# Kernel tuning notes

Hardware: AMD Instinct MI355X
Metric: run time of the kernel (lower is better)

## Reference

```python
import jax, jax.numpy as jnp
from jax import lax
import numpy as np

B, C, H, W = 8, 192, 56, 56
N = H * W
K_CLUSTERS = 16   # num_centroids
K_NBRS = 9        # kNN neighbors
FACTOR = 2
COUT = C * FACTOR # hidden channels of graph conv
CPE_K = 7         # depthwise CPE kernel (odd)


def setup_inputs() -> dict:
    key = jax.random.key(0)
    ks = jax.random.split(key, 12)
    s = 0.02
    return {
        "x": jax.random.normal(ks[0], (B, C, H, W), jnp.float32),
        "labels": jax.random.randint(ks[1], (B, N), 0, K_CLUSTERS, jnp.int32),
        "cpe_w": jax.random.normal(ks[2], (C, 1, CPE_K, CPE_K), jnp.float32) * s,
        "cpe_b": jnp.zeros((C,), jnp.float32),
        "fc1_w": jax.random.normal(ks[3], (C, C), jnp.float32) * s,
        "fc1_b": jnp.zeros((C,), jnp.float32),
        "nn_v_w": jax.random.normal(ks[4], (2 * C, COUT), jnp.float32) * s,
        "nn_v_b": jnp.zeros((COUT,), jnp.float32),
        "nn_c_w": jax.random.normal(ks[5], (2 * C, COUT), jnp.float32) * s,
        "nn_c_b": jnp.zeros((COUT,), jnp.float32),
        "fc2_w": jax.random.normal(ks[6], (COUT, C), jnp.float32) * s,
        "fc2_b": jnp.zeros((C,), jnp.float32),
    }


def reference(x, labels, cpe_w, cpe_b, fc1_w, fc1_b, nn_v_w, nn_v_b,
              nn_c_w, nn_c_b, fc2_w, fc2_b):
    Bx, Cx, Hx, Wx = x.shape
    n = Hx * Wx
    shortcut = x
    # --- Conditional Position Encoding: depthwise conv + residual ---
    pe = lax.conv_general_dilated(
        x, cpe_w, (1, 1), "SAME", feature_group_count=Cx,
        dimension_numbers=("NCHW", "OIHW", "NCHW"))
    x = pe + cpe_b[None, :, None, None] + x
    # --- fc1: 1x1 conv ---
    xf = jnp.einsum("bchw,cd->bdhw", x, fc1_w) + fc1_b[None, :, None, None]
    xn = xf.reshape(Bx, Cx, n).transpose(0, 2, 1)  # [B,N,C]
    # --- organize_and_map: stable sort nodes by cluster label ---
    order = jnp.argsort(labels, axis=1)            # sorted pos -> orig idx (stable)
    mapping = jnp.argsort(order, axis=1)           # orig idx -> sorted pos
    xs = jnp.take_along_axis(xn, order[:, :, None], axis=1)  # [B,N,C]
    ls = jnp.take_along_axis(labels, order, axis=1)          # [B,N]
    # --- kNN on l2-normalized feats, restricted to same cluster ---
    xe = xs / jnp.maximum(jnp.linalg.norm(xs, axis=-1, keepdims=True), 1e-12)
    sq = jnp.sum(xe * xe, axis=-1)                 # [B,N]
    d2 = sq[:, :, None] + sq[:, None, :] - 2.0 * jnp.einsum("bnc,bmc->bnm", xe, xe)
    same = ls[:, :, None] == ls[:, None, :]        # [B,N,N] cluster mask
    d2 = jnp.where(same, d2, jnp.inf)
    _, nbr = lax.top_k(-d2, K_NBRS)                # [B,N,k] nearest in-cluster
    valid = jnp.take_along_axis(same, nbr, axis=2) # False when cluster < k
    # --- vertex edge conv: max_j MLP([x_i, x_j - x_i]) ---
    xj = jax.vmap(lambda xb, nb: xb[nb])(xs, nbr)  # [B,N,k,C]
    xi = xs[:, :, None, :]
    msg = jnp.concatenate([jnp.broadcast_to(xi, xj.shape), xj - xi], axis=-1)
    h = jax.nn.gelu(msg @ nn_v_w + nn_v_b)         # [B,N,k,COUT]
    h = jnp.where(valid[..., None], h, -jnp.inf)   # self is always valid
    hv = jnp.max(h, axis=2)                        # [B,N,COUT]
    # --- centroid edge conv over cluster centers (fully connected per image) ---
    onehot = (ls[:, :, None] == jnp.arange(K_CLUSTERS)[None, None, :]).astype(xs.dtype)
    cnt = jnp.maximum(onehot.sum(axis=1), 1.0)     # [B,K]
    cen = jnp.einsum("bnk,bnc->bkc", onehot, xs) / cnt[:, :, None]
    ci = cen[:, :, None, :]
    cj = cen[:, None, :, :]
    cmsg = jnp.concatenate(
        [jnp.broadcast_to(ci, (Bx, K_CLUSTERS, K_CLUSTERS, Cx)), cj - ci], axis=-1)
    hc = jnp.max(jax.nn.gelu(cmsg @ nn_c_w + nn_c_b), axis=2)  # [B,K,COUT]
    hcn = jax.vmap(lambda hb, lb: hb[lb])(hc, ls)  # scatter center feat to nodes
    hn = hv + hcn                                  # [B,N,COUT]
    # --- unshuffle back to original raster order ---
    out_nodes = jnp.take_along_axis(hn, mapping[:, :, None], axis=1)
    # --- fc2: 1x1 conv back to C, residual ---
    y = out_nodes @ fc2_w + fc2_b                  # [B,N,C]
    y = y.transpose(0, 2, 1).reshape(Bx, Cx, Hx, Wx)
    return y + shortcut
```

## Files before the change

kernel.cpp:

```cpp
#include <hip/hip_runtime.h>
#include <math.h>

#define NB 8
#define NC 192
#define NH 56
#define NW 56
#define NN 3136
#define NK 16
#define KNB 9
#define NCOUT 384
#define LPMAX 320
#define DSTRIDE 320
#define DSLOT (320 * 320)

#define FLT_INF __builtin_inff()

typedef short s16x8 __attribute__((ext_vector_type(8)));
typedef _Float16 f16x8 __attribute__((ext_vector_type(8)));
typedef float f32x4 __attribute__((ext_vector_type(4)));
typedef unsigned short us8 __attribute__((ext_vector_type(8)));
typedef unsigned short us4 __attribute__((ext_vector_type(4)));

__device__ __forceinline__ float gelu_t(float x) {
    const float k0 = 0.7978845608028654f;
    float u = k0 * (x + 0.044715f * x * x * x);
    float sg = __builtin_amdgcn_rcpf(1.0f + __expf(-2.0f * u));
    return x * sg;
}

__device__ __forceinline__ unsigned short f2bf(float f) {
    unsigned u = __float_as_uint(f);
    u += 0x7fff + ((u >> 16) & 1);
    return (unsigned short)(u >> 16);
}

__device__ __forceinline__ float bf2f(unsigned short h) {
    return __uint_as_float(((unsigned)h) << 16);
}

#define FRONT_CONV_BLOCKS (NB * NC)
#define FRONT_ORDER_BLOCKS (NB * NK)
#define FRONT_WCVT_BLOCKS 288
__global__ __launch_bounds__(256) void front_kernel(
    const float* __restrict__ X, const float* __restrict__ W7, const float* __restrict__ bias,
    unsigned short* __restrict__ xpe,
    const int* __restrict__ labels, int* __restrict__ order, int* __restrict__ mapping,
    int* __restrict__ lsv, int* __restrict__ cntk, int* __restrict__ offk,
    const float* __restrict__ Wf1, const float* __restrict__ Wv, const float* __restrict__ Wf2,
    unsigned short* __restrict__ wf1, unsigned short* __restrict__ wfpmq,
    unsigned short* __restrict__ wfq, unsigned short* __restrict__ wf2) {
    __shared__ float tile[62 * 62];
    __shared__ float wl[49];
    int bid = blockIdx.x;
    int tid = threadIdx.x;
    if (bid < FRONT_CONV_BLOCKS) {
        int bc = bid;
        int c = bc % NC;
        const float* Xp = X + (size_t)bc * NN;
        if (tid < 49) wl[tid] = W7[(size_t)c * 49 + tid];
        for (int idx = tid; idx < 62 * 62; idx += 256) {
            int ty = idx / 62, tx = idx % 62;
            int gy = ty - 3, gx = tx - 3;
            float v = 0.0f;
            if (gy >= 0 && gy < NH && gx >= 0 && gx < NW) v = Xp[gy * NW + gx];
            tile[idx] = v;
        }
        __syncthreads();
        float cb = bias[c];
        for (int g = tid; g < (NN / 4); g += 256) {
            int y = g / (NW / 4), x0 = (g % (NW / 4)) * 4;
            float a0 = 0.f, a1 = 0.f, a2 = 0.f, a3 = 0.f;
#pragma unroll
            for (int dy = 0; dy < 7; ++dy) {
                const float* tr = &tile[(y + dy) * 62 + x0];
#pragma unroll
                for (int dx = 0; dx < 7; ++dx) {
                    float wv = wl[dy * 7 + dx];
                    a0 += tr[dx] * wv;
                    a1 += tr[dx + 1] * wv;
                    a2 += tr[dx + 2] * wv;
                    a3 += tr[dx + 3] * wv;
                }
            }
            const float* rr = &tile[(y + 3) * 62 + x0 + 3];
            us4 o;
            o[0] = f2bf(a0 + cb + rr[0]);
            o[1] = f2bf(a1 + cb + rr[1]);
            o[2] = f2bf(a2 + cb + rr[2]);
            o[3] = f2bf(a3 + cb + rr[3]);
            *(us4*)(xpe + (size_t)bc * NN + y * NW + x0) = o;
        }
    } else if (bid < FRONT_CONV_BLOCKS + FRONT_ORDER_BLOCKS) {
        if (tid >= 64) return;
        int idx = bid - FRONT_CONV_BLOCKS;
        int b = idx >> 4;
        int k = idx & 15;
        int lane = tid;
        const int* lb = labels + (size_t)b * NN;
        int cntLess = 0, cntEq = 0;
        for (int n0 = 0; n0 < NN; n0 += 64) {
            int lab = lb[n0 + lane] & 15;
            cntLess += __popcll(__ballot(lab < k));
            cntEq += __popcll(__ballot(lab == k));
        }
        int base = cntLess;
        int run = 0;
        for (int n0 = 0; n0 < NN; n0 += 64) {
            int n = n0 + lane;
            int lab = lb[n] & 15;
            bool p = (lab == k);
            unsigned long long mask = __ballot(p);
            int rank = __popcll(mask & ((1ull << lane) - 1ull));
            if (p) {
                int pos = base + run + rank;
                order[b * NN + pos] = n;
                mapping[b * NN + n] = pos;
                lsv[b * NN + pos] = k;
            }
            run += __popcll(mask);
        }
        if (lane == 0) {
            offk[b * NK + k] = base;
            cntk[b * NK + k] = cntEq;
        }
    } else {
        int u = bid - (FRONT_CONV_BLOCKS + FRONT_ORDER_BLOCKS);
        int nt = u % 6, kc = (u / 6) % 12, z = u / 72;
        const float* W;
        unsigned short* Bf;
        int ldw, rowoff, KC, NT;
        bool diff = false;
        if (z == 0) { W = Wf1; Bf = wf1; ldw = NC; rowoff = 0; KC = 6; NT = 3; }
        else if (z == 1) { W = Wv; Bf = wfpmq; ldw = NCOUT; rowoff = 0; KC = 6; NT = 6; diff = true; }
        else if (z == 2) { W = Wv; Bf = wfq; ldw = NCOUT; rowoff = NC; KC = 6; NT = 6; }
        else { W = Wf2; Bf = wf2; ldw = NC; rowoff = 0; KC = 12; NT = 3; }
        if (nt >= NT || kc >= KC) return;
        int c = tid >> 6, l = tid & 63;
        int n = l & 15, q = l >> 4;
        int col = nt * 64 + c * 16 + n;
        int krow = rowoff + kc * 32 + q * 8;
        unsigned short pack[8];
#pragma unroll
        for (int j = 0; j < 8; ++j) {
            float v = W[(size_t)(krow + j) * ldw + col];
            if (diff) v -= W[(size_t)(NC + krow + j) * ldw + col];
            pack[j] = f2bf(v);
        }
        *(us8*)(Bf + ((((size_t)nt * KC + kc) * 4 + c) * 64 + l) * 8) = *(const us8*)pack;
    }
}

__global__ __launch_bounds__(256) void tcvt_kernel(const unsigned short* __restrict__ xpe,
                                                   unsigned short* __restrict__ Af) {
    __shared__ unsigned short t[32][72];
    int b = blockIdx.z, kc = blockIdx.y, n0 = blockIdx.x * 64;
    int tid = threadIdx.x;
    int cl = tid >> 3, nl = (tid & 7) * 8;
    const unsigned short* src = xpe + ((size_t)b * NC + kc * 32 + cl) * NN + n0 + nl;
    *(us8*)&t[cl][nl] = *(const us8*)src;
    __syncthreads();
    int w = tid >> 6, l = tid & 63;
    int m = l & 15, q = l >> 4;
    int nloc = w * 16 + m;
    unsigned short pack[8];
#pragma unroll
    for (int j = 0; j < 8; ++j) pack[j] = t[q * 8 + j][nloc];
    int sg = blockIdx.x * 4 + w;
    *(us8*)(Af + (size_t)b * NN * NC + (((size_t)sg * 6 + kc) * 64 + l) * 8) =
        *(const us8*)pack;
}

template <int KC>
__global__ __launch_bounds__(256) void gemm_mfma(const unsigned short* __restrict__ Af,
                                                 size_t aStride,
                                                 const unsigned short* __restrict__ Bf,
                                                 const float* __restrict__ bias,
                                                 float* __restrict__ C, size_t cStride,
                                                 int ldc, unsigned short* __restrict__ Cfrag,
                                                 const int* __restrict__ rowmap) {
    int b = blockIdx.z;
    int w = threadIdx.x >> 6, lane = threadIdx.x & 63;
    int sg = blockIdx.y * 4 + w;
    int n0 = blockIdx.x * 64;
    const unsigned short* Ap = Af + (size_t)b * aStride + ((size_t)sg * KC * 64 + lane) * 8;
    const unsigned short* Bp = Bf + ((size_t)blockIdx.x * KC * 256 + lane) * 8;
    f32x4 acc[4] = {};
#pragma unroll
    for (int kc = 0; kc < KC; ++kc) {
        s16x8 a = *(const s16x8*)(Ap + kc * 512);
#pragma unroll
        for (int c = 0; c < 4; ++c) {
            s16x8 bv = *(const s16x8*)(Bp + kc * 2048 + c * 512);
            acc[c] = __builtin_amdgcn_mfma_f32_16x16x32_bf16(a, bv, acc[c], 0, 0, 0);
        }
    }
    int col0 = lane & 15, rq = lane >> 4;
    float* Cb = C + (size_t)b * cStride;
    int kcd = ldc >> 5;
#pragma unroll
    for (int r = 0; r < 4; ++r) {
        int grow = sg * 16 + rq * 4 + r;
        int orow = rowmap ? rowmap[(size_t)b * NN + grow] : grow;
#pragma unroll
        for (int c = 0; c < 4; ++c) {
            int col = n0 + c * 16 + col0;
            float v = acc[c][r];
            if (bias) v += bias[col];
            Cb[(size_t)orow * ldc + col] = v;
            if (Cfrag) {
                int s2 = orow >> 4, m2 = orow & 15;
                int kc2 = col >> 5, q2 = (col >> 3) & 3, j2 = col & 7;
                Cfrag[(size_t)b * cStride +
                      (((size_t)s2 * kcd + kc2) * 64 + q2 * 16 + m2) * 8 + j2] = f2bf(v);
            }
        }
    }
}

template <int KC>
__global__ __launch_bounds__(256) void gemm_mfma_pq(const unsigned short* __restrict__ Af,
                                                    size_t aStride,
                                                    const unsigned short* __restrict__ B1,
                                                    const unsigned short* __restrict__ B2,
                                                    const float* __restrict__ bias,
                                                    unsigned short* __restrict__ PmQ,
                                                    unsigned short* __restrict__ Qh,
                                                    size_t cStride, int ldc) {
    int b = blockIdx.z;
    int w = threadIdx.x >> 6, lane = threadIdx.x & 63;
    int sg = blockIdx.y * 4 + w;
    int n0 = blockIdx.x * 64;
    const unsigned short* Ap = Af + (size_t)b * aStride + ((size_t)sg * KC * 64 + lane) * 8;
    const unsigned short* Bp1 = B1 + ((size_t)blockIdx.x * KC * 256 + lane) * 8;
    const unsigned short* Bp2 = B2 + ((size_t)blockIdx.x * KC * 256 + lane) * 8;
    f32x4 acc1[4] = {};
    f32x4 acc2[4] = {};
#pragma unroll
    for (int kc = 0; kc < KC; ++kc) {
        s16x8 a = *(const s16x8*)(Ap + kc * 512);
#pragma unroll
        for (int c = 0; c < 4; ++c) {
            s16x8 b1 = *(const s16x8*)(Bp1 + kc * 2048 + c * 512);
            acc1[c] = __builtin_amdgcn_mfma_f32_16x16x32_bf16(a, b1, acc1[c], 0, 0, 0);
            s16x8 b2 = *(const s16x8*)(Bp2 + kc * 2048 + c * 512);
            acc2[c] = __builtin_amdgcn_mfma_f32_16x16x32_bf16(a, b2, acc2[c], 0, 0, 0);
        }
    }
    int col0 = lane & 15, rq = lane >> 4;
    unsigned short* Pb = PmQ + (size_t)b * cStride;
    unsigned short* Qb = Qh + (size_t)b * cStride;
#pragma unroll
    for (int r = 0; r < 4; ++r) {
        int grow = sg * 16 + rq * 4 + r;
#pragma unroll
        for (int c = 0; c < 4; ++c) {
            int col = n0 + c * 16 + col0;
            Pb[(size_t)grow * ldc + col] = f2bf(acc1[c][r] + bias[col]);
            Qb[(size_t)grow * ldc + col] = f2bf(acc2[c][r]);
        }
    }
}

template <int KC>
__global__ __launch_bounds__(256) void gemm_mfma_hb(const unsigned short* __restrict__ Af,
                                                    size_t aStride,
                                                    const unsigned short* __restrict__ Bf,
                                                    const float* __restrict__ bias,
                                                    unsigned short* __restrict__ C,
                                                    size_t cStride, int ldc,
                                                    const int* __restrict__ rowmap) {
    int b = blockIdx.z;
    int w = threadIdx.x >> 6, lane = threadIdx.x & 63;
    int sg = blockIdx.y * 4 + w;
    int n0 = blockIdx.x * 64;
    const unsigned short* Ap = Af + (size_t)b * aStride + ((size_t)sg * KC * 64 + lane) * 8;
    const unsigned short* Bp = Bf + ((size_t)blockIdx.x * KC * 256 + lane) * 8;
    f32x4 acc[4] = {};
#pragma unroll
    for (int kc = 0; kc < KC; ++kc) {
        s16x8 a = *(const s16x8*)(Ap + kc * 512);
#pragma unroll
        for (int c = 0; c < 4; ++c) {
            s16x8 bv = *(const s16x8*)(Bp + kc * 2048 + c * 512);
            acc[c] = __builtin_amdgcn_mfma_f32_16x16x32_bf16(a, bv, acc[c], 0, 0, 0);
        }
    }
    int col0 = lane & 15, rq = lane >> 4;
    unsigned short* Cb = C + (size_t)b * cStride;
#pragma unroll
    for (int r = 0; r < 4; ++r) {
        int grow = sg * 16 + rq * 4 + r;
        int orow = rowmap[(size_t)b * NN + grow];
#pragma unroll
        for (int c = 0; c < 4; ++c) {
            int col = n0 + c * 16 + col0;
            Cb[(size_t)orow * ldc + col] = f2bf(acc[c][r] + bias[col]);
        }
    }
}

__global__ __launch_bounds__(384) void xe_cvt_kernel(const float* __restrict__ xs,
                                                     const int* __restrict__ offk,
                                                     const int* __restrict__ cntk,
                                                     _Float16* __restrict__ xef,
                                                     float* __restrict__ sqv) {
    __shared__ float psum[16][25];
    __shared__ float rloc[16];
    int b = blockIdx.z, k = blockIdx.y, strip = blockIdx.x;
    int bk = b * NK + k;
    int base = offk[bk], L = cntk[bk];
    if (strip * 16 >= L) return;
    int kc = threadIdx.x >> 6, l = threadIdx.x & 63;
    int m = l & 15, q = l >> 4;
    int rl = strip * 16 + m;
    int row = base + (rl < L ? rl : L - 1);
    const float* src = xs + ((size_t)b * NN + row) * NC + kc * 32 + q * 8;
    float4 v0 = *(const float4*)src;
    float4 v1 = *(const float4*)(src + 4);
    float part = v0.x * v0.x + v0.y * v0.y + v0.z * v0.z + v0.w * v0.w + v1.x * v1.x +
                 v1.y * v1.y + v1.z * v1.z + v1.w * v1.w;
    psum[m][kc * 4 + q] = part;
    __syncthreads();
    if (threadIdx.x < 16) {
        float s = 0.0f;
#pragma unroll
        for (int i2 = 0; i2 < 24; ++i2) s += psum[threadIdx.x][i2];
        float nrm = fmaxf(sqrtf(s), 1e-12f);
        float ri = 1.0f / nrm;
        rloc[threadIdx.x] = ri;
        if (strip * 16 + (int)threadIdx.x < L)
            sqv[(size_t)b * NN + base + strip * 16 + threadIdx.x] = (s * ri) * ri;
    }
    __syncthreads();
    float rv = rloc[m];
    f16x8 pack;
    pack[0] = (_Float16)(v0.x * rv);
    pack[1] = (_Float16)(v0.y * rv);
    pack[2] = (_Float16)(v0.z * rv);
    pack[3] = (_Float16)(v0.w * rv);
    pack[4] = (_Float16)(v1.x * rv);
    pack[5] = (_Float16)(v1.y * rv);
    pack[6] = (_Float16)(v1.z * rv);
    pack[7] = (_Float16)(v1.w * rv);
    *(f16x8*)(xef + (size_t)bk * (20 * 6 * 512) + (((size_t)strip * 6 + kc) * 64 + l) * 8) =
        pack;
}

__global__ __launch_bounds__(256) void gram_kernel(const _Float16* __restrict__ xef,
                                                   const float* __restrict__ sqv,
                                                   const int* __restrict__ offk,
                                                   const int* __restrict__ cntk,
                                                   float* __restrict__ D) {
    int bk = blockIdx.z;
    int b = bk >> 4;
    int base = offk[bk], L = cntk[bk];
    int ti = blockIdx.x, tj = blockIdx.y;
    if (ti * 64 >= L || tj * 64 >= L) return;
    int w = threadIdx.x >> 6, lane = threadIdx.x & 63;
    const _Float16* Xf = xef + (size_t)bk * (20 * 6 * 512);
    const _Float16* Ap = Xf + (((size_t)(ti * 4 + w) * 6) * 64 + lane) * 8;
    f32x4 acc[4] = {};
#pragma unroll
    for (int kc = 0; kc < 6; ++kc) {
        f16x8 a = *(const f16x8*)(Ap + kc * 512);
#pragma unroll
        for (int js = 0; js < 4; ++js) {
            f16x8 bv = *(const f16x8*)(Xf + (((size_t)(tj * 4 + js) * 6 + kc) * 64 + lane) * 8);
            acc[js] = __builtin_amdgcn_mfma_f32_16x16x32_f16(a, bv, acc[js], 0, 0, 0);
        }
    }
    float* Dr = D + (size_t)bk * DSLOT;
    const float* Sb = sqv + (size_t)b * NN + base;
    int col0 = lane & 15, rq = lane >> 4;
#pragma unroll
    for (int r = 0; r < 4; ++r) {
        int i = ti * 64 + w * 16 + rq * 4 + r;
        if (i >= L) continue;
        float si = Sb[i];
#pragma unroll
        for (int js = 0; js < 4; ++js) {
            int j = tj * 64 + js * 16 + col0;
            if (j < L) Dr[(size_t)i * DSTRIDE + j] = si + Sb[j] - 2.0f * acc[js][r];
        }
    }
}

#define LEXLT(da, ca, db, cb) ((da) < (db) || ((da) == (db) && (ca) < (cb)))
__global__ __launch_bounds__(256) void select9_kernel(const float* __restrict__ D,
                                                      const int* __restrict__ lsv,
                                                      const int* __restrict__ offk,
                                                      const int* __restrict__ cntk,
                                                      int* __restrict__ nbr) {
    int b = blockIdx.y;
    int r = blockIdx.x * 4 + (threadIdx.x >> 6);
    int lane = threadIdx.x & 63;
    int k = lsv[(size_t)b * NN + r];
    int bk = b * NK + k;
    int base = offk[bk], L = cntk[bk];
    int Lc = L < LPMAX ? L : LPMAX;
    const float* Dr = D + (size_t)bk * DSLOT + (size_t)(r - base) * DSTRIDE;
    float d0, d1, d2, d3, d4;
    int c0, c1, c2, c3, c4;
    c0 = lane;
    c1 = lane + 64;
    c2 = lane + 128;
    c3 = lane + 192;
    c4 = lane + 256;
    d0 = c0 < Lc ? Dr[c0] : FLT_INF;
    d1 = c1 < Lc ? Dr[c1] : FLT_INF;
    d2 = c2 < Lc ? Dr[c2] : FLT_INF;
    d3 = c3 < Lc ? Dr[c3] : FLT_INF;
    d4 = c4 < Lc ? Dr[c4] : FLT_INF;
#define CS(da, ca, db, cb)                  \
    if (LEXLT(db, cb, da, ca)) {            \
        float t = da; da = db; db = t;      \
        int u = ca; ca = cb; cb = u;        \
    }
    CS(d0, c0, d1, c1) CS(d3, c3, d4, c4) CS(d2, c2, d4, c4) CS(d2, c2, d3, c3)
    CS(d1, c1, d4, c4) CS(d0, c0, d3, c3) CS(d0, c0, d2, c2) CS(d1, c1, d3, c3)
    CS(d1, c1, d2, c2)
#undef CS
    size_t row = (size_t)b * NN + r;
    for (int q = 0; q < KNB; ++q) {
        float bd = d0;
        int bc = c0;
#pragma unroll
        for (int m = 32; m; m >>= 1) {
            float od = __shfl_xor(bd, m, 64);
            int oc = __shfl_xor(bc, m, 64);
            if (LEXLT(od, oc, bd, bc)) {
                bd = od;
                bc = oc;
            }
        }
        if (lane == 0) nbr[row * KNB + q] = base + bc;
        if (d0 == bd && c0 == bc) {
            d0 = d1; c0 = c1;
            d1 = d2; c1 = c2;
            d2 = d3; c2 = c3;
            d3 = d4; c3 = c4;
            d4 = FLT_INF; c4 = 0x7fffffff;
        }
    }
}

__global__ __launch_bounds__(768) void cenpq_kernel(const float* __restrict__ xs,
                                                    const int* __restrict__ offk,
                                                    const int* __restrict__ cntk,
                                                    const float* __restrict__ Wc,
                                                    const float* __restrict__ bc,
                                                    float* __restrict__ Pc,
                                                    float* __restrict__ Qc) {
    __shared__ float part[4][NC];
    __shared__ float ce[NC];
    __shared__ float pcs[NCOUT], qcs[NCOUT];
    int bk = blockIdx.x;
    int b = bk >> 4;
    int base = offk[bk], L = cntk[bk];
    int w = threadIdx.x / NC;
    int c = threadIdx.x % NC;
    const float* Xb = xs + ((size_t)b * NN + base) * NC + c;
    float s = 0.0f;
    for (int r = w; r < L; r += 4) s += Xb[(size_t)r * NC];
    part[w][c] = s;
    __syncthreads();
    if (threadIdx.x < NC) {
        int cc = threadIdx.x;
        float tot = part[0][cc] + part[1][cc] + part[2][cc] + part[3][cc];
        ce[cc] = tot / fmaxf((float)L, 1.0f);
    }
    __syncthreads();
    int o = threadIdx.x % NCOUT, half = threadIdx.x / NCOUT;
    float pc = 0.0f, qc = 0.0f;
    int cs = half * 96, cend = cs + 96;
    for (int c2 = cs; c2 < cend; ++c2) {
        float cv = ce[c2];
        pc += cv * Wc[(size_t)c2 * NCOUT + o];
        qc += cv * Wc[(size_t)(NC + c2) * NCOUT + o];
    }
    if (half == 1) {
        pcs[o] = pc;
        qcs[o] = qc;
    }
    __syncthreads();
    if (half == 0) {
        Pc[(size_t)bk * NCOUT + o] = pc + pcs[o] + bc[o];
        Qc[(size_t)bk * NCOUT + o] = qc + qcs[o];
    }
}

__global__ __launch_bounds__(384) void hcmax_kernel(const float* __restrict__ Pc,
                                                    const float* __restrict__ Qc,
                                                    float* __restrict__ hc) {
    int b = blockIdx.x >> 4, i = blockIdx.x & 15;
    int o = threadIdx.x;
    float pi = Pc[((size_t)b * NK + i) * NCOUT + o];
    float qi = Qc[((size_t)b * NK + i) * NCOUT + o];
    float pmq = pi - qi;
    float qmn = FLT_INF, qmx = -FLT_INF;
    for (int j = 0; j < NK; ++j) {
        float v = Qc[((size_t)b * NK + j) * NCOUT + o];
        qmn = fminf(qmn, v);
        qmx = fmaxf(qmx, v);
    }
    hc[((size_t)b * NK + i) * NCOUT + o] =
        fmaxf(gelu_t(pmq + qmn), gelu_t(pmq + qmx));
}

__global__ __launch_bounds__(192) void hv_kernel(const unsigned short* __restrict__ PmQ,
                                                 const unsigned short* __restrict__ Qh,
                                                 const int* __restrict__ nbr,
                                                 const int* __restrict__ lsv,
                                                 const float* __restrict__ hc,
                                                 unsigned short* __restrict__ hnf) {
    int b = blockIdx.y;
    int t = threadIdx.x;
    int rsub = t / 48, c = t % 48;
    int i = blockIdx.x * 4 + rsub;
    size_t row = (size_t)b * NN + i;
    int lab = lsv[row];
    int o0 = c * 8;
    int jn[KNB];
#pragma unroll
    for (int q = 0; q < KNB; ++q) jn[q] = nbr[row * KNB + q];
    const unsigned short* Qbb = Qh + (size_t)b * NN * NCOUT + o0;
    us8 pv = *(const us8*)(PmQ + row * NCOUT + o0);
    us8 q0 = *(const us8*)(Qbb + (size_t)jn[0] * NCOUT);
    float qmn[8], qmx[8];
#pragma unroll
    for (int e = 0; e < 8; ++e) {
        float v = bf2f(q0[e]);
        qmn[e] = v;
        qmx[e] = v;
    }
#pragma unroll
    for (int q = 1; q < KNB; ++q) {
        us8 qv = *(const us8*)(Qbb + (size_t)jn[q] * NCOUT);
#pragma unroll
        for (int e = 0; e < 8; ++e) {
            float v = bf2f(qv[e]);
            qmn[e] = fminf(qmn[e], v);
            qmx[e] = fmaxf(qmx[e], v);
        }
    }
    const float* hcr = hc + ((size_t)b * NK + lab) * NCOUT + o0;
    float4 h0 = *(const float4*)hcr;
    float4 h1 = *(const float4*)(hcr + 4);
    float hcv[8] = {h0.x, h0.y, h0.z, h0.w, h1.x, h1.y, h1.z, h1.w};
    unsigned short pack[8];
#pragma unroll
    for (int e = 0; e < 8; ++e) {
        float pmq = bf2f(pv[e]);
        float m = fmaxf(gelu_t(pmq + qmn[e]), gelu_t(pmq + qmx[e]));
        pack[e] = f2bf(m + hcv[e]);
    }
    int s = i >> 4, mm = i & 15;
    *(us8*)(hnf + (size_t)b * NN * NCOUT +
            (((size_t)s * 12 + (c >> 2)) * 64 + (c & 3) * 16 + mm) * 8) = *(const us8*)pack;
}

__global__ void out_kernel(const unsigned short* __restrict__ T, const float* __restrict__ X,
                           float* __restrict__ Y) {
    __shared__ float t[32][33];
    int b = blockIdx.z;
    int n0 = blockIdx.y * 32, c0 = blockIdx.x * 32;
    int tx = threadIdx.x, ty = threadIdx.y;
#pragma unroll
    for (int q = 0; q < 4; ++q) {
        int n = n0 + ty + q * 8;
        t[ty + q * 8][tx] = bf2f(T[((size_t)b * NN + n) * NC + c0 + tx]);
    }
    __syncthreads();
#pragma unroll
    for (int q = 0; q < 4; ++q) {
        int c = c0 + ty + q * 8;
        size_t idx = ((size_t)b * NC + c) * NN + n0 + tx;
        Y[idx] = t[tx][ty + q * 8] + X[idx];
    }
}

extern "C" void kernel_launch(void* const* d_in, const int* in_sizes, int n_in, void* d_out,
                              int out_size, void* d_ws, size_t ws_size, hipStream_t stream) {
    const float* x = (const float*)d_in[0];
    const int* labels = (const int*)d_in[1];
    const float* cpe_w = (const float*)d_in[2];
    const float* cpe_b = (const float*)d_in[3];
    const float* fc1_w = (const float*)d_in[4];
    const float* fc1_b = (const float*)d_in[5];
    const float* nn_v_w = (const float*)d_in[6];
    const float* nn_v_b = (const float*)d_in[7];
    const float* nn_c_w = (const float*)d_in[8];
    const float* nn_c_b = (const float*)d_in[9];
    const float* fc2_w = (const float*)d_in[10];
    const float* fc2_b = (const float*)d_in[11];
    float* out = (float*)d_out;

    const size_t SZ_XS = (size_t)NB * NN * NC;
    const size_t SZ_P = (size_t)NB * NN * NCOUT;
    const size_t BN = (size_t)NB * NN;
    const size_t SZ_CEN = (size_t)NB * NK * NC;
    const size_t SZ_PC = (size_t)NB * NK * NCOUT;

    float* base = (float*)d_ws;
    float* xs = base;
    float* xpeRegion = xs + SZ_XS;
    float* Pb = xpeRegion + SZ_XS;
    float* Qb = Pb + SZ_P;
    float* rinv = Qb + SZ_P;
    float* sqv = rinv + BN;
    float* cen = sqv + BN;
    float* Pc = cen + SZ_CEN;
    float* Qc = Pc + SZ_PC;
    float* hcv = Qc + SZ_PC;
    int* order = (int*)(hcv + SZ_PC);
    int* mapping = order + BN;
    int* lsv = mapping + BN;
    int* nbrv = lsv + BN;
    int* cntk = nbrv + BN * KNB;
    int* offk = cntk + NB * NK;
    unsigned short* xpe = (unsigned short*)xpeRegion;
    float* Dbuf = Pb;
    unsigned short* PmQh = (unsigned short*)Pb;
    unsigned short* Qh = (unsigned short*)Qb;
    unsigned short* out_t = (unsigned short*)xs;
    unsigned short* frag = (unsigned short*)(offk + NB * NK);
    unsigned short* xpeT_frag = frag;
    unsigned short* xs_frag = frag + SZ_XS;
    unsigned short* hn_frag = frag;
    unsigned short* wf1 = frag + 2 * SZ_XS;
    unsigned short* wfpmq = wf1 + (size_t)NC * NC;
    unsigned short* wfq = wfpmq + (size_t)NC * NCOUT;
    unsigned short* wf2 = wfq + (size_t)NC * NCOUT;
    _Float16* xef = (_Float16*)(wf2 + (size_t)NCOUT * NC);

    front_kernel<<<FRONT_CONV_BLOCKS + FRONT_ORDER_BLOCKS + FRONT_WCVT_BLOCKS, 256, 0, stream>>>(
        x, cpe_w, cpe_b, xpe, labels, order, mapping, lsv, cntk, offk, fc1_w, nn_v_w, fc2_w,
        wf1, wfpmq, wfq, wf2);
    tcvt_kernel<<<dim3(NN / 64, NC / 32, NB), 256, 0, stream>>>(xpe, xpeT_frag);
    gemm_mfma<6><<<dim3(NC / 64, NN / 64, NB), 256, 0, stream>>>(
        xpeT_frag, SZ_XS / NB, wf1, fc1_b, xs, (size_t)NN * NC, NC, xs_frag, mapping);
    xe_cvt_kernel<<<dim3(LPMAX / 16, NK, NB), 384, 0, stream>>>(xs, offk, cntk, xef, sqv);
    gram_kernel<<<dim3(LPMAX / 64, LPMAX / 64, NB * NK), 256, 0, stream>>>(xef, sqv, offk,
                                                                           cntk, Dbuf);
    select9_kernel<<<dim3(NN / 4, NB), 256, 0, stream>>>(Dbuf, lsv, offk, cntk, nbrv);
    gemm_mfma_pq<6><<<dim3(NCOUT / 64, NN / 64, NB), 256, 0, stream>>>(
        xs_frag, SZ_XS / NB, wfpmq, wfq, nn_v_b, PmQh, Qh, (size_t)NN * NCOUT, NCOUT);
    cenpq_kernel<<<NB * NK, 768, 0, stream>>>(xs, offk, cntk, nn_c_w, nn_c_b, Pc, Qc);
    hcmax_kernel<<<NB * NK, NCOUT, 0, stream>>>(Pc, Qc, hcv);
    hv_kernel<<<dim3(NN / 4, NB), 192, 0, stream>>>(PmQh, Qh, nbrv, lsv, hcv, hn_frag);
    gemm_mfma_hb<12><<<dim3(NC / 64, NN / 64, NB), 256, 0, stream>>>(
        hn_frag, SZ_P / NB, wf2, fc2_b, out_t, (size_t)NN * NC, NC, order);
    out_kernel<<<dim3(NC / 32, NN / 32, NB), dim3(32, 8), 0, stream>>>(out_t, x, out);
}
```

Baseline: 297.1 us.

## Interleave batch index across blocks and move unshuffle gather into output kernel

Every kernel now linearizes its grid and takes the batch index from the low three bits, so consecutive blocks work on different images. This likely aims to spread the uneven per-cluster work evenly across the XCDs/CUs. The fc2 GEMM also writes rows in sorted order, and the output kernel does the unshuffle by reading through the mapping array. That replaces a scattered store with a gathered load. The index math adds a small cost per block, and gemm_mfma hardcodes 49 row-blocks in its decode.

```diff
diff --git a/kernel.cpp b/kernel.cpp
--- a/kernel.cpp
+++ b/kernel.cpp
@@ -37,6 +37,7 @@
 __device__ __forceinline__ float bf2f(unsigned short h) {
     return __uint_as_float(((unsigned)h) << 16);
 }
+
 
 #define FRONT_CONV_BLOCKS (NB * NC)
 #define FRONT_ORDER_BLOCKS (NB * NK)
@@ -54,7 +55,7 @@
     int bid = blockIdx.x;
     int tid = threadIdx.x;
     if (bid < FRONT_CONV_BLOCKS) {
-        int bc = bid;
+        int bc = (bid & 7) * NC + (bid >> 3);
         int c = bc % NC;
         const float* Xp = X + (size_t)bc * NN;
         if (tid < 49) wl[tid] = W7[(size_t)c * 49 + tid];
@@ -153,7 +154,10 @@
 __global__ __launch_bounds__(256) void tcvt_kernel(const unsigned short* __restrict__ xpe,
                                                    unsigned short* __restrict__ Af) {
     __shared__ unsigned short t[32][72];
-    int b = blockIdx.z, kc = blockIdx.y, n0 = blockIdx.x * 64;
+    int lin = ((int)blockIdx.z * 6 + blockIdx.y) * 49 + blockIdx.x;
+    int b = lin & 7, pos = lin >> 3;
+    int kc = pos / 49, nx = pos % 49;
+    int n0 = nx * 64;
     int tid = threadIdx.x;
     int cl = tid >> 3, nl = (tid & 7) * 8;
     const unsigned short* src = xpe + ((size_t)b * NC + kc * 32 + cl) * NN + n0 + nl;
@@ -165,7 +169,7 @@
     unsigned short pack[8];
 #pragma unroll
     for (int j = 0; j < 8; ++j) pack[j] = t[q * 8 + j][nloc];
-    int sg = blockIdx.x * 4 + w;
+    int sg = nx * 4 + w;
     *(us8*)(Af + (size_t)b * NN * NC + (((size_t)sg * 6 + kc) * 64 + l) * 8) =
         *(const us8*)pack;
 }
@@ -178,12 +182,15 @@
                                                  float* __restrict__ C, size_t cStride,
                                                  int ldc, unsigned short* __restrict__ Cfrag,
                                                  const int* __restrict__ rowmap) {
-    int b = blockIdx.z;
+    int NX = gridDim.x;
+    int lin = ((int)blockIdx.z * 49 + blockIdx.y) * NX + blockIdx.x;
+    int b = lin & 7, pos = lin >> 3;
+    int bx = pos % NX, by = pos / NX;
     int w = threadIdx.x >> 6, lane = threadIdx.x & 63;
-    int sg = blockIdx.y * 4 + w;
-    int n0 = blockIdx.x * 64;
+    int sg = by * 4 + w;
+    int n0 = bx * 64;
     const unsigned short* Ap = Af + (size_t)b * aStride + ((size_t)sg * KC * 64 + lane) * 8;
-    const unsigned short* Bp = Bf + ((size_t)blockIdx.x * KC * 256 + lane) * 8;
+    const unsigned short* Bp = Bf + ((size_t)bx * KC * 256 + lane) * 8;
     f32x4 acc[4] = {};
 #pragma unroll
     for (int kc = 0; kc < KC; ++kc) {
@@ -226,13 +233,15 @@
                                                     unsigned short* __restrict__ PmQ,
                                                     unsigned short* __restrict__ Qh,
                                                     size_t cStride, int ldc) {
-    int b = blockIdx.z;
+    int lin = ((int)blockIdx.z * 49 + blockIdx.y) * 6 + blockIdx.x;
+    int b = lin & 7, pos = lin >> 3;
+    int bx = pos % 6, by = pos / 6;
     int w = threadIdx.x >> 6, lane = threadIdx.x & 63;
-    int sg = blockIdx.y * 4 + w;
-    int n0 = blockIdx.x * 64;
+    int sg = by * 4 + w;
+    int n0 = bx * 64;
     const unsigned short* Ap = Af + (size_t)b * aStride + ((size_t)sg * KC * 64 + lane) * 8;
-    const unsigned short* Bp1 = B1 + ((size_t)blockIdx.x * KC * 256 + lane) * 8;
-    const unsigned short* Bp2 = B2 + ((size_t)blockIdx.x * KC * 256 + lane) * 8;
+    const unsigned short* Bp1 = B1 + ((size_t)bx * KC * 256 + lane) * 8;
+    const unsigned short* Bp2 = B2 + ((size_t)bx * KC * 256 + lane) * 8;
     f32x4 acc1[4] = {};
     f32x4 acc2[4] = {};
 #pragma unroll
@@ -267,14 +276,15 @@
                                                     const unsigned short* __restrict__ Bf,
                                                     const float* __restrict__ bias,
                                                     unsigned short* __restrict__ C,
-                                                    size_t cStride, int ldc,
-                                                    const int* __restrict__ rowmap) {
-    int b = blockIdx.z;
+                                                    size_t cStride, int ldc) {
+    int lin = ((int)blockIdx.z * 49 + blockIdx.y) * 3 + blockIdx.x;
+    int b = lin & 7, pos = lin >> 3;
+    int bx = pos % 3, by = pos / 3;
     int w = threadIdx.x >> 6, lane = threadIdx.x & 63;
-    int sg = blockIdx.y * 4 + w;
-    int n0 = blockIdx.x * 64;
+    int sg = by * 4 + w;
+    int n0 = bx * 64;
     const unsigned short* Ap = Af + (size_t)b * aStride + ((size_t)sg * KC * 64 + lane) * 8;
-    const unsigned short* Bp = Bf + ((size_t)blockIdx.x * KC * 256 + lane) * 8;
+    const unsigned short* Bp = Bf + ((size_t)bx * KC * 256 + lane) * 8;
     f32x4 acc[4] = {};
 #pragma unroll
     for (int kc = 0; kc < KC; ++kc) {
@@ -290,11 +300,10 @@
 #pragma unroll
     for (int r = 0; r < 4; ++r) {
         int grow = sg * 16 + rq * 4 + r;
-        int orow = rowmap[(size_t)b * NN + grow];
 #pragma unroll
         for (int c = 0; c < 4; ++c) {
             int col = n0 + c * 16 + col0;
-            Cb[(size_t)orow * ldc + col] = f2bf(acc[c][r] + bias[col]);
+            Cb[(size_t)grow * ldc + col] = f2bf(acc[c][r] + bias[col]);
         }
     }
 }
@@ -306,7 +315,9 @@
                                                      float* __restrict__ sqv) {
     __shared__ float psum[16][25];
     __shared__ float rloc[16];
-    int b = blockIdx.z, k = blockIdx.y, strip = blockIdx.x;
+    int lin = ((int)blockIdx.z * 16 + blockIdx.y) * 20 + blockIdx.x;
+    int b = lin & 7, pos = lin >> 3;
+    int k = pos / 20, strip = pos % 20;
     int bk = b * NK + k;
     int base = offk[bk], L = cntk[bk];
     if (strip * 16 >= L) return;
@@ -351,10 +362,12 @@
                                                    const int* __restrict__ offk,
                                                    const int* __restrict__ cntk,
                                                    float* __restrict__ D) {
-    int bk = blockIdx.z;
-    int b = bk >> 4;
+    int lin = ((int)blockIdx.z * 5 + blockIdx.y) * 5 + blockIdx.x;
+    int b = lin & 7, pos = lin >> 3;
+    int k = pos / 25, rr = pos % 25;
+    int tj = rr / 5, ti = rr % 5;
+    int bk = b * NK + k;
     int base = offk[bk], L = cntk[bk];
-    int ti = blockIdx.x, tj = blockIdx.y;
     if (ti * 64 >= L || tj * 64 >= L) return;
     int w = threadIdx.x >> 6, lane = threadIdx.x & 63;
     const _Float16* Xf = xef + (size_t)bk * (20 * 6 * 512);
@@ -391,8 +404,9 @@
                                                       const int* __restrict__ offk,
                                                       const int* __restrict__ cntk,
                                                       int* __restrict__ nbr) {
-    int b = blockIdx.y;
-    int r = blockIdx.x * 4 + (threadIdx.x >> 6);
+    int lin = (int)blockIdx.y * 784 + blockIdx.x;
+    int b = lin & 7, quad = lin >> 3;
+    int r = quad * 4 + (threadIdx.x >> 6);
     int lane = threadIdx.x & 63;
     int k = lsv[(size_t)b * NN + r];
     int bk = b * NK + k;
@@ -454,7 +468,7 @@
     __shared__ float part[4][NC];
     __shared__ float ce[NC];
     __shared__ float pcs[NCOUT], qcs[NCOUT];
-    int bk = blockIdx.x;
+    int bk = ((int)blockIdx.x & 7) * NK + ((int)blockIdx.x >> 3);
     int b = bk >> 4;
     int base = offk[bk], L = cntk[bk];
     int w = threadIdx.x / NC;
@@ -492,7 +506,8 @@
 __global__ __launch_bounds__(384) void hcmax_kernel(const float* __restrict__ Pc,
                                                     const float* __restrict__ Qc,
                                                     float* __restrict__ hc) {
-    int b = blockIdx.x >> 4, i = blockIdx.x & 15;
+    int bk = ((int)blockIdx.x & 7) * NK + ((int)blockIdx.x >> 3);
+    int b = bk >> 4, i = bk & 15;
     int o = threadIdx.x;
     float pi = Pc[((size_t)b * NK + i) * NCOUT + o];
     float qi = Qc[((size_t)b * NK + i) * NCOUT + o];
@@ -513,10 +528,11 @@
                                                  const int* __restrict__ lsv,
                                                  const float* __restrict__ hc,
                                                  unsigned short* __restrict__ hnf) {
-    int b = blockIdx.y;
+    int lin = (int)blockIdx.y * 784 + blockIdx.x;
+    int b = lin & 7, quad = lin >> 3;
     int t = threadIdx.x;
     int rsub = t / 48, c = t % 48;
-    int i = blockIdx.x * 4 + rsub;
+    int i = quad * 4 + rsub;
     size_t row = (size_t)b * NN + i;
     int lab = lsv[row];
     int o0 = c * 8;
@@ -560,15 +576,17 @@
 }
 
 __global__ void out_kernel(const unsigned short* __restrict__ T, const float* __restrict__ X,
-                           float* __restrict__ Y) {
+                           const int* __restrict__ mapping, float* __restrict__ Y) {
     __shared__ float t[32][33];
-    int b = blockIdx.z;
-    int n0 = blockIdx.y * 32, c0 = blockIdx.x * 32;
+    int lin = ((int)blockIdx.z * 98 + blockIdx.y) * 6 + blockIdx.x;
+    int b = lin & 7, pos = lin >> 3;
+    int c0 = (pos % 6) * 32, n0 = (pos / 6) * 32;
     int tx = threadIdx.x, ty = threadIdx.y;
 #pragma unroll
     for (int q = 0; q < 4; ++q) {
         int n = n0 + ty + q * 8;
-        t[ty + q * 8][tx] = bf2f(T[((size_t)b * NN + n) * NC + c0 + tx]);
+        int srow = mapping[(size_t)b * NN + n];
+        t[ty + q * 8][tx] = bf2f(T[((size_t)b * NN + srow) * NC + c0 + tx]);
     }
     __syncthreads();
 #pragma unroll
@@ -649,6 +667,6 @@
     hcmax_kernel<<<NB * NK, NCOUT, 0, stream>>>(Pc, Qc, hcv);
     hv_kernel<<<dim3(NN / 4, NB), 192, 0, stream>>>(PmQh, Qh, nbrv, lsv, hcv, hn_frag);
     gemm_mfma_hb<12><<<dim3(NC / 64, NN / 64, NB), 256, 0, stream>>>(
-        hn_frag, SZ_P / NB, wf2, fc2_b, out_t, (size_t)NN * NC, NC, order);
-    out_kernel<<<dim3(NC / 32, NN / 32, NB), dim3(32, 8), 0, stream>>>(out_t, x, out);
-}
+        hn_frag, SZ_P / NB, wf2, fc2_b, out_t, (size_t)NN * NC, NC);
+    out_kernel<<<dim3(NC / 32, NN / 32, NB), dim3(32, 8), 0, stream>>>(out_t, x, mapping, out);
+}
```

Result: faster. 284.0 us (-4.4%).
